# Performance work log

Measured on AMD Instinct MI355X. Metric: run time of the kernel, lower is better.

The kernel has to match this reference:

```python
import jax, jax.numpy as jnp
import numpy as np
from jax import lax

B, L, F = 32, 2048, 76   # batch, seq_len, feat_dim
H = 128                  # conv hidden channels
D = 128                  # prototype dim (last 1x1 conv)
P = 128                  # number of prototypes
CLASS_SIZE = 2


def setup_inputs() -> dict:
    key = jax.random.key(0)
    ks = jax.random.split(key, 8)
    w = lambda k, shape: jax.random.normal(k, shape, jnp.float32) * 0.05
    return {
        "x": jax.random.normal(ks[0], (B, L, F), jnp.float32),
        "W1": w(ks[1], (H, F, 5)), "b1": jnp.zeros((H,), jnp.float32),
        "W2": w(ks[2], (H, H, 5)), "b2": jnp.zeros((H,), jnp.float32),
        "W3": w(ks[3], (H, H, 5)), "b3": jnp.zeros((H,), jnp.float32),
        "Wo1": w(ks[4], (D, H)), "bo1": jnp.zeros((D,), jnp.float32),
        "Wo2": w(ks[5], (D, D)), "bo2": jnp.zeros((D,), jnp.float32),
        "prototypes": jax.random.uniform(ks[6], (P, D), jnp.float32),
        "protop_classes": jnp.concatenate([jnp.zeros(P // 2, jnp.int32), jnp.ones(P // 2, jnp.int32)]),
    }


def _conv1d_same(h, W, b):
    # h: (B, C, L), W: (O, C, K=5), symmetric padding 2 == torch padding=k//2
    y = lax.conv_general_dilated(h, W, window_strides=(1,), padding=[(2, 2)],
                                 dimension_numbers=("NCW", "OIW", "NCW"))
    return y + b[None, :, None]


def _maxpool2(h):
    return lax.reduce_window(h, -jnp.inf, lax.max, (1, 1, 2), (1, 1, 2), "VALID")


def reference(x, W1, b1, W2, b2, W3, b3, Wo1, bo1, Wo2, bo2, prototypes, protop_classes):
    h = jnp.transpose(x, (0, 2, 1))  # (B, F, L)
    for W, b in ((W1, b1), (W2, b2), (W3, b3)):
        h = _maxpool2(jax.nn.relu(_conv1d_same(h, W, b)))
    # 1x1 convs as channel matmuls
    h = jax.nn.relu(jnp.einsum("bcl,oc->bol", h, Wo1) + bo1[None, :, None])
    h = jax.nn.relu(jnp.einsum("bcl,oc->bol", h, Wo2) + bo2[None, :, None])
    f = jnp.transpose(h, (0, 2, 1))  # (B, Lp=256, D)
    # l2_conv via ||a-b||^2 = ||a||^2 - 2 a.b + ||b||^2 (same math, GEMM form)
    d2 = (jnp.sum(f * f, axis=-1, keepdims=True)
          - 2.0 * jnp.einsum("bld,pd->blp", f, prototypes)
          + jnp.sum(prototypes * prototypes, axis=-1))  # (B, Lp, P)
    dis = jnp.sqrt(jnp.maximum(d2, 1e-12))
    min_dis = jnp.min(dis, axis=1)  # (B, P): min over patches
    # dis2sim, 'log' activation
    sim = jnp.log((min_dis + 1.0) / (min_dis + 1e-4))
    # init_weights: last_layer.weight[i,j] = 1 if protop_classes[j]==i else -0.5
    lw = jnp.where(protop_classes[None, :] == jnp.arange(CLASS_SIZE)[:, None], 1.0, -0.5)
    out = jax.nn.sigmoid(sim @ lw.T)  # (B, CLASS_SIZE)
    return out, min_dis
```

## Files before the change

kernel.cpp:

```cpp
#include <hip/hip_runtime.h>
#include <cmath>


typedef __attribute__((ext_vector_type(8))) short short8;
typedef __attribute__((ext_vector_type(4))) float f32x4;

__device__ __forceinline__ unsigned short f2bf(float v) {
    union { float f; unsigned u; } x; x.f = v;
    unsigned r = x.u + 0x7fffu + ((x.u >> 16) & 1u);
    return (unsigned short)(r >> 16);
}
__device__ __forceinline__ float bf2f(unsigned short b) {
    union { unsigned u; float f; } x; x.u = ((unsigned)b) << 16;
    return x.f;
}

__device__ void pack_conv_w(int t, int total, const float* __restrict__ W, int C,
                            unsigned short* __restrict__ dst)
{
    if (t >= total) return;
    int lane = t & 63, rest = t >> 6;
    int mf = rest & 7; rest >>= 3;
    int kk = rest % 5, cc = rest / 5;
    int m = mf * 16 + (lane & 15);
    int cb = cc * 32 + (lane >> 4) * 8;
    unsigned short v[8];
#pragma unroll
    for (int j = 0; j < 8; ++j) {
        int c = cb + j;
        v[j] = (c < C) ? f2bf(W[((size_t)m * C + c) * 5 + kk]) : (unsigned short)0;
    }
    *(uint4*)&dst[(size_t)t * 8] = *(uint4*)v;
}

__device__ void pack_mat(int t, const float* __restrict__ M, unsigned short* __restrict__ dst)
{
    if (t >= 2048) return;
    int lane = t & 63, mf = (t >> 6) & 7, cc = t >> 9;
    int m = mf * 16 + (lane & 15);
    int c0 = cc * 32 + (lane >> 4) * 8;
    unsigned short v[8];
#pragma unroll
    for (int j = 0; j < 8; ++j) v[j] = f2bf(M[(size_t)m * 128 + c0 + j]);
    *(uint4*)&dst[(size_t)t * 8] = *(uint4*)v;
}

__global__ __launch_bounds__(256)
void prep_weights_kernel(const float* __restrict__ W1, const float* __restrict__ W2,
                         const float* __restrict__ W3, const float* __restrict__ Wo1,
                         const float* __restrict__ Wo2, const float* __restrict__ protos,
                         unsigned short* A1, unsigned short* A2, unsigned short* A3,
                         unsigned short* AW1, unsigned short* AW2, unsigned short* AP,
                         float* pn, unsigned* pm_bits, unsigned* cnt)
{
    int t = blockIdx.x * 256 + threadIdx.x;
    switch (blockIdx.y) {
    case 0: pack_conv_w(t, 7680,  W1, 76,  A1); break;
    case 1: pack_conv_w(t, 10240, W2, 128, A2); break;
    case 2: pack_conv_w(t, 10240, W3, 128, A3); break;
    case 3: pack_mat(t, Wo1, AW1); break;
    case 4: pack_mat(t, Wo2, AW2); break;
    case 5: pack_mat(t, protos, AP); break;
    case 6:
        if (t < 128) {
            float s = 0.f;
            for (int d = 0; d < 128; ++d) {
                float v = bf2f(f2bf(protos[(size_t)t * 128 + d]));
                s = fmaf(v, v, s);
            }
            pn[t] = s;
        }
        break;
    case 7:
        if (t < 4096)                    pm_bits[t] = 0x7F800000u;
        else if (cnt && t < 4128)        cnt[t - 4096] = 0u;
        break;
    }
}

template <int MF, int NJ, int NCC, int STRIDE, int ROWMAX>
__device__ __forceinline__ void conv_k(const unsigned short* __restrict__ Af,
                                       const unsigned short* __restrict__ sIn,
                                       int nbase, int mf0, int lane,
                                       f32x4 (&acc)[MF][NJ])
{
    const int lc = lane & 15;
    const int lk = (lane >> 4) * 8;
    constexpr int NSTEP = NCC * 5;
#pragma unroll
    for (int i = 0; i < MF; ++i)
#pragma unroll
        for (int j = 0; j < NJ; ++j) acc[i][j] = (f32x4){0.f, 0.f, 0.f, 0.f};

    short8 a_cur[MF], a_nxt[MF];
#pragma unroll
    for (int i = 0; i < MF; ++i)
        a_cur[i] = *(const short8*)&Af[(((size_t)mf0 + i) * 64 + lane) * 8];

#pragma unroll
    for (int step = 0; step < NSTEP; ++step) {
        const int kk = step % 5, cc = step / 5;
        if (step + 1 < NSTEP) {
#pragma unroll
            for (int i = 0; i < MF; ++i)
                a_nxt[i] = *(const short8*)&Af[(((size_t)(step + 1) * 8 + mf0 + i) * 64 + lane) * 8];
        }
        short8 bb[NJ];
#pragma unroll
        for (int j = 0; j < NJ; ++j) {
            int row = nbase + j * 16 + lc + kk;
            if (ROWMAX >= 0) row = min(row, ROWMAX);
            bb[j] = *(const short8*)&sIn[row * STRIDE + cc * 32 + lk];
        }
        __builtin_amdgcn_s_setprio(1);
#pragma unroll
        for (int j = 0; j < NJ; ++j)
#pragma unroll
            for (int i = 0; i < MF; ++i)
                acc[i][j] = __builtin_amdgcn_mfma_f32_16x16x32_bf16(a_cur[i], bb[j], acc[i][j], 0, 0, 0);
        __builtin_amdgcn_s_setprio(0);
#pragma unroll
        for (int i = 0; i < MF; ++i) a_cur[i] = a_nxt[i];
    }
}

__device__ __forceinline__ void gemm_head(const unsigned short* __restrict__ Af,
                                          const unsigned short* __restrict__ s_in,
                                          int mf0h, int lane, f32x4 (&acc)[2])
{
    const int lc = lane & 15;
    const int lk = (lane >> 4) * 8;
    acc[0] = (f32x4){0.f, 0.f, 0.f, 0.f};
    acc[1] = (f32x4){0.f, 0.f, 0.f, 0.f};
#pragma unroll
    for (int cc = 0; cc < 4; ++cc) {
        short8 a[2];
#pragma unroll
        for (int i = 0; i < 2; ++i)
            a[i] = *(const short8*)&Af[(((size_t)cc * 8 + mf0h + i) * 64 + lane) * 8];
        short8 bb = *(const short8*)&s_in[lc * 136 + cc * 32 + lk];
        __builtin_amdgcn_s_setprio(1);
#pragma unroll
        for (int i = 0; i < 2; ++i)
            acc[i] = __builtin_amdgcn_mfma_f32_16x16x32_bf16(a[i], bb, acc[i], 0, 0, 0);
        __builtin_amdgcn_s_setprio(0);
    }
}

__global__ __launch_bounds__(256, 4)
void mega_kernel(const float* __restrict__ x,
                 const unsigned short* __restrict__ A1, const float* __restrict__ b1,
                 const unsigned short* __restrict__ A2, const float* __restrict__ b2,
                 const unsigned short* __restrict__ A3, const float* __restrict__ b3,
                 const unsigned short* __restrict__ AW1, const float* __restrict__ bo1,
                 const unsigned short* __restrict__ AW2, const float* __restrict__ bo2,
                 const unsigned short* __restrict__ AP,  const float* __restrict__ pn,
                 unsigned* __restrict__ pm_bits, unsigned* __restrict__ cnt,
                 const int* __restrict__ classes, float* __restrict__ out)
{
    __shared__ __align__(16) unsigned short s_x[100 * 104];
    __shared__ __align__(16) unsigned short s_h1[44 * 136];
    __shared__ float s_cb[768];
    __shared__ float s_part[64];
    __shared__ unsigned s_last;
    unsigned short* s_h2 = s_x;
    unsigned short* s_f  = s_x + 2720;
    unsigned short* s_t1 = s_x + 4896;

    const int tid  = threadIdx.x;
    const int u    = blockIdx.x;
    const int b    = blockIdx.y;
    const int lane = tid & 63;
    const int wid  = tid >> 6;
    const int mg   = wid & 1;
    const int ng   = wid >> 1;
    const int mf0  = mg * 4;
    const int lc   = lane & 15;
    const int lq   = (lane >> 4) * 4;

    for (int i = tid; i < 768; i += 256) {
        const float* src = (i < 128) ? b1 : (i < 256) ? b2 : (i < 384) ? b3
                         : (i < 512) ? bo1 : (i < 640) ? bo2 : pn;
        s_cb[i] = src[i & 127];
    }

    const int xbase = 64 * u - 14;
    for (int idx = tid; idx < 100 * 24; idx += 256) {
        int pos = idx / 24, c0 = (idx % 24) * 4;
        int l = xbase + pos;
        unsigned short v[4] = {0, 0, 0, 0};
        if (c0 < 76 && l >= 0 && l < 2048) {
            float4 xv = *(const float4*)&x[((size_t)b * 2048 + l) * 76 + c0];
            v[0] = f2bf(xv.x); v[1] = f2bf(xv.y); v[2] = f2bf(xv.z); v[3] = f2bf(xv.w);
        }
        *(uint2*)&s_x[pos * 104 + c0] = *(uint2*)v;
    }
    __syncthreads();

    {
        f32x4 acc[4][3];
        conv_k<4, 3, 3, 104, -1>(A1, s_x, ng * 48, mf0, lane, acc);

#pragma unroll
        for (int i = 0; i < 4; ++i) {
            const int ch0 = (mf0 + i) * 16 + lq;
#pragma unroll
            for (int j = 0; j < 3; ++j) {
                const int nl = ng * 48 + j * 16 + lc;
                unsigned short pk[4];
#pragma unroll
                for (int r = 0; r < 4; ++r) {
                    float v = fmaxf(acc[i][j][r] + s_cb[ch0 + r], 0.f);
                    float o = __shfl_xor(v, 1);
                    pk[r] = f2bf(fmaxf(v, o));
                }
                if ((lc & 1) == 0) {
                    int rr = nl >> 1;
                    int jg = 32 * u - 6 + rr;
                    if (rr < 44) {
                        uint2 val = (jg >= 0 && jg < 1024) ? *(uint2*)pk : make_uint2(0u, 0u);
                        *(uint2*)&s_h1[rr * 136 + ch0] = val;
                    }
                }
            }
        }
    }
    __syncthreads();

    {
        if (tid < 136) ((uint4*)(s_f + 8 * 136))[tid] = make_uint4(0u, 0u, 0u, 0u);

        f32x4 acc[2][3];
        conv_k<2, 3, 4, 136, 43>(A2, s_h1, 0, wid * 2, lane, acc);

#pragma unroll
        for (int i = 0; i < 2; ++i) {
            const int ch0 = (wid * 2 + i) * 16 + lq;
#pragma unroll
            for (int j = 0; j < 3; ++j) {
                const int nl = j * 16 + lc;
                unsigned short pk[4];
#pragma unroll
                for (int r = 0; r < 4; ++r) {
                    float v = fmaxf(acc[i][j][r] + s_cb[128 + ch0 + r], 0.f);
                    float o = __shfl_xor(v, 1);
                    pk[r] = f2bf(fmaxf(v, o));
                }
                if ((lc & 1) == 0) {
                    int rr = nl >> 1;
                    int jg = 16 * u - 2 + rr;
                    if (rr < 20) {
                        uint2 val = (jg >= 0 && jg < 512) ? *(uint2*)pk : make_uint2(0u, 0u);
                        *(uint2*)&s_h2[rr * 136 + ch0] = val;
                    }
                }
            }
        }
    }
    __syncthreads();

    {
        f32x4 acc[2][1];
        conv_k<2, 1, 4, 136, -1>(A3, s_h2, 0, wid * 2, lane, acc);

#pragma unroll
        for (int i = 0; i < 2; ++i) {
            const int ch0 = (wid * 2 + i) * 16 + lq;
            unsigned short pk[4];
#pragma unroll
            for (int r = 0; r < 4; ++r) {
                float v = fmaxf(acc[i][0][r] + s_cb[256 + ch0 + r], 0.f);
                float o = __shfl_xor(v, 1);
                pk[r] = f2bf(fmaxf(v, o));
            }
            if ((lc & 1) == 0)
                *(uint2*)&s_f[(lc >> 1) * 136 + ch0] = *(uint2*)pk;
        }
    }
    __syncthreads();

    const int mf0h = wid * 2;
    f32x4 hacc[2];

    gemm_head(AW1, s_f, mf0h, lane, hacc);
#pragma unroll
    for (int i = 0; i < 2; ++i) {
        const int ch0 = (mf0h + i) * 16 + lq;
        unsigned short pk[4];
#pragma unroll
        for (int r = 0; r < 4; ++r)
            pk[r] = f2bf(fmaxf(hacc[i][r] + s_cb[384 + ch0 + r], 0.f));
        *(uint2*)&s_t1[lc * 136 + ch0] = *(uint2*)pk;
    }
    __syncthreads();

    gemm_head(AW2, s_t1, mf0h, lane, hacc);
    {
        float fnp = 0.f;
#pragma unroll
        for (int i = 0; i < 2; ++i) {
            const int ch0 = (mf0h + i) * 16 + lq;
            unsigned short pk[4];
#pragma unroll
            for (int r = 0; r < 4; ++r) {
                float v = fmaxf(hacc[i][r] + s_cb[512 + ch0 + r], 0.f);
                fnp = fmaf(v, v, fnp);
                pk[r] = f2bf(v);
            }
            *(uint2*)&s_f[lc * 136 + ch0] = *(uint2*)pk;
        }
        fnp += __shfl_xor(fnp, 16);
        fnp += __shfl_xor(fnp, 32);
        if (lane < 16) s_part[wid * 16 + lc] = fnp;
    }
    __syncthreads();

    gemm_head(AP, s_f, mf0h, lane, hacc);
    const float fn_l = s_part[lc] + s_part[16 + lc] + s_part[32 + lc] + s_part[48 + lc];

#pragma unroll
    for (int i = 0; i < 2; ++i) {
#pragma unroll
        for (int r = 0; r < 4; ++r) {
            const int p = (mf0h + i) * 16 + lq + r;
            float d2 = fn_l + s_cb[640 + p] - 2.f * hacc[i][r];
            float m = sqrtf(fmaxf(d2, 1e-12f));
#pragma unroll
            for (int s = 1; s < 8; s <<= 1)
                m = fminf(m, __shfl_xor(m, s));
            if (lc == 0)
                atomicMin(&pm_bits[(size_t)b * 128 + p], __float_as_uint(m));
        }
    }

    if (cnt) {
        __syncthreads();
        if (tid == 0) {
            __threadfence();
            s_last = atomicAdd(&cnt[b], 1u);
        }
        __syncthreads();
        if (s_last == 31u) {
            __threadfence();
            float* r0 = (float*)s_h1;
            float* r1 = r0 + 128;
            if (tid < 128) {
                unsigned mb = atomicOr(&pm_bits[(size_t)b * 128 + tid], 0u);
                float m = __uint_as_float(mb);
                out[64 + b * 128 + tid] = m;
                float sim = logf((m + 1.0f) / (m + 1e-4f));
                int c = classes[tid];
                r0[tid] = (c == 0) ? sim : -0.5f * sim;
                r1[tid] = (c == 1) ? sim : -0.5f * sim;
            }
            __syncthreads();
            for (int s = 64; s > 0; s >>= 1) {
                if (tid < s) { r0[tid] += r0[tid + s]; r1[tid] += r1[tid + s]; }
                __syncthreads();
            }
            if (tid == 0) {
                out[b * 2 + 0] = 1.f / (1.f + expf(-r0[0]));
                out[b * 2 + 1] = 1.f / (1.f + expf(-r1[0]));
            }
        }
    }
}

__global__ __launch_bounds__(128)
void finalize_kernel(const float* __restrict__ pm,
                     const int* __restrict__ classes,
                     float* __restrict__ out)
{
    __shared__ float r0[128], r1[128];
    const int b = blockIdx.x, p = threadIdx.x;
    float m = pm[(size_t)b * 128 + p];
    out[64 + b * 128 + p] = m;

    float sim = logf((m + 1.0f) / (m + 1e-4f));
    int cls = classes[p];
    r0[p] = (cls == 0) ? sim : -0.5f * sim;
    r1[p] = (cls == 1) ? sim : -0.5f * sim;
    __syncthreads();
    for (int s = 64; s > 0; s >>= 1) {
        if (p < s) { r0[p] += r0[p + s]; r1[p] += r1[p + s]; }
        __syncthreads();
    }
    if (p == 0) {
        out[b * 2 + 0] = 1.f / (1.f + expf(-r0[0]));
        out[b * 2 + 1] = 1.f / (1.f + expf(-r1[0]));
    }
}

extern "C" void kernel_launch(void* const* d_in, const int* in_sizes, int n_in,
                              void* d_out, int out_size, void* d_ws, size_t ws_size,
                              hipStream_t stream)
{
    (void)in_sizes; (void)n_in; (void)out_size;
    const float* x    = (const float*)d_in[0];
    const float* W1   = (const float*)d_in[1];
    const float* b1   = (const float*)d_in[2];
    const float* W2   = (const float*)d_in[3];
    const float* b2   = (const float*)d_in[4];
    const float* W3   = (const float*)d_in[5];
    const float* b3   = (const float*)d_in[6];
    const float* Wo1  = (const float*)d_in[7];
    const float* bo1  = (const float*)d_in[8];
    const float* Wo2  = (const float*)d_in[9];
    const float* bo2  = (const float*)d_in[10];
    const float* prot = (const float*)d_in[11];
    const int*   cls  = (const int*)d_in[12];
    float* out = (float*)d_out;

    char* ws = (char*)d_ws;
    unsigned short* A1  = (unsigned short*)(ws);
    unsigned short* A2  = (unsigned short*)(ws + 122880);
    unsigned short* A3  = (unsigned short*)(ws + 286720);
    unsigned short* AW1 = (unsigned short*)(ws + 450560);
    unsigned short* AW2 = (unsigned short*)(ws + 483328);
    unsigned short* AP  = (unsigned short*)(ws + 516096);
    float*          pn  = (float*)(ws + 548864);
    unsigned*       pm  = (unsigned*)(ws + 549376);
    const bool merged = (ws_size >= 565760u + 128u);
    unsigned*       cnt = merged ? (unsigned*)(ws + 565760) : nullptr;

    prep_weights_kernel<<<dim3(40, 8), 256, 0, stream>>>(W1, W2, W3, Wo1, Wo2, prot,
                                                         A1, A2, A3, AW1, AW2, AP, pn, pm, cnt);
    mega_kernel<<<dim3(32, 32), 256, 0, stream>>>(x, A1, b1, A2, b2, A3, b3,
                                                  AW1, bo1, AW2, bo2, AP, pn, pm, cnt,
                                                  cls, out);
    if (!merged)
        finalize_kernel<<<32, 128, 0, stream>>>((const float*)pm, cls, out);
}
```

Before: 152.6 us.

## Retile conv1 warps over channels only and drop A-fragment prefetch and setprio

Conv1 work is split so each wave handles 2 channel fragments across all 96 positions (MF=2, NJ=6) instead of 4 channel fragments across half the positions. This halves per-wave weight-fragment traffic for conv1 but doubles LDS B reads per MFMA. The software double-buffering of A fragments and the s_setprio hints are removed, and the cc loop is no longer fully unrolled, which lowers register pressure but may expose global-load latency.

```diff
diff --git a/kernel.cpp b/kernel.cpp
--- a/kernel.cpp
+++ b/kernel.cpp
@@ -86,41 +86,32 @@
 {
     const int lc = lane & 15;
     const int lk = (lane >> 4) * 8;
-    constexpr int NSTEP = NCC * 5;
 #pragma unroll
     for (int i = 0; i < MF; ++i)
 #pragma unroll
         for (int j = 0; j < NJ; ++j) acc[i][j] = (f32x4){0.f, 0.f, 0.f, 0.f};
 
-    short8 a_cur[MF], a_nxt[MF];
-#pragma unroll
-    for (int i = 0; i < MF; ++i)
-        a_cur[i] = *(const short8*)&Af[(((size_t)mf0 + i) * 64 + lane) * 8];
-
-#pragma unroll
-    for (int step = 0; step < NSTEP; ++step) {
-        const int kk = step % 5, cc = step / 5;
-        if (step + 1 < NSTEP) {
+    for (int cc = 0; cc < NCC; ++cc) {
+#pragma unroll
+        for (int kk = 0; kk < 5; ++kk) {
+            const int step = cc * 5 + kk;
+            short8 a[MF];
 #pragma unroll
             for (int i = 0; i < MF; ++i)
-                a_nxt[i] = *(const short8*)&Af[(((size_t)(step + 1) * 8 + mf0 + i) * 64 + lane) * 8];
-        }
-        short8 bb[NJ];
-#pragma unroll
-        for (int j = 0; j < NJ; ++j) {
-            int row = nbase + j * 16 + lc + kk;
-            if (ROWMAX >= 0) row = min(row, ROWMAX);
-            bb[j] = *(const short8*)&sIn[row * STRIDE + cc * 32 + lk];
-        }
-        __builtin_amdgcn_s_setprio(1);
-#pragma unroll
-        for (int j = 0; j < NJ; ++j)
-#pragma unroll
-            for (int i = 0; i < MF; ++i)
-                acc[i][j] = __builtin_amdgcn_mfma_f32_16x16x32_bf16(a_cur[i], bb[j], acc[i][j], 0, 0, 0);
-        __builtin_amdgcn_s_setprio(0);
-#pragma unroll
-        for (int i = 0; i < MF; ++i) a_cur[i] = a_nxt[i];
+                a[i] = *(const short8*)&Af[(((size_t)step * 8 + mf0 + i) * 64 + lane) * 8];
+            short8 bb[NJ];
+#pragma unroll
+            for (int j = 0; j < NJ; ++j) {
+                int row = nbase + j * 16 + lc + kk;
+                if (ROWMAX >= 0) row = min(row, ROWMAX);
+                bb[j] = *(const short8*)&sIn[row * STRIDE + cc * 32 + lk];
+            }
+#pragma unroll
+            for (int j = 0; j < NJ; ++j)
+#pragma unroll
+                for (int i = 0; i < MF; ++i)
+                    acc[i][j] = __builtin_amdgcn_mfma_f32_16x16x32_bf16(a[i], bb[j], acc[i][j], 0, 0, 0);
+        }
     }
 }
 
@@ -139,11 +130,9 @@
         for (int i = 0; i < 2; ++i)
             a[i] = *(const short8*)&Af[(((size_t)cc * 8 + mf0h + i) * 64 + lane) * 8];
         short8 bb = *(const short8*)&s_in[lc * 136 + cc * 32 + lk];
-        __builtin_amdgcn_s_setprio(1);
 #pragma unroll
         for (int i = 0; i < 2; ++i)
             acc[i] = __builtin_amdgcn_mfma_f32_16x16x32_bf16(a[i], bb, acc[i], 0, 0, 0);
-        __builtin_amdgcn_s_setprio(0);
     }
 }
 
@@ -172,9 +161,7 @@
     const int b    = blockIdx.y;
     const int lane = tid & 63;
     const int wid  = tid >> 6;
-    const int mg   = wid & 1;
-    const int ng   = wid >> 1;
-    const int mf0  = mg * 4;
+    const int mf0  = wid * 2;
     const int lc   = lane & 15;
     const int lq   = (lane >> 4) * 4;
 
@@ -198,15 +185,15 @@
     __syncthreads();
 
     {
-        f32x4 acc[4][3];
-        conv_k<4, 3, 3, 104, -1>(A1, s_x, ng * 48, mf0, lane, acc);
-
-#pragma unroll
-        for (int i = 0; i < 4; ++i) {
+        f32x4 acc[2][6];
+        conv_k<2, 6, 3, 104, -1>(A1, s_x, 0, mf0, lane, acc);
+
+#pragma unroll
+        for (int i = 0; i < 2; ++i) {
             const int ch0 = (mf0 + i) * 16 + lq;
 #pragma unroll
-            for (int j = 0; j < 3; ++j) {
-                const int nl = ng * 48 + j * 16 + lc;
+            for (int j = 0; j < 6; ++j) {
+                const int nl = j * 16 + lc;
                 unsigned short pk[4];
 #pragma unroll
                 for (int r = 0; r < 4; ++r) {
@@ -231,11 +218,11 @@
         if (tid < 136) ((uint4*)(s_f + 8 * 136))[tid] = make_uint4(0u, 0u, 0u, 0u);
 
         f32x4 acc[2][3];
-        conv_k<2, 3, 4, 136, 43>(A2, s_h1, 0, wid * 2, lane, acc);
+        conv_k<2, 3, 4, 136, 43>(A2, s_h1, 0, mf0, lane, acc);
 
 #pragma unroll
         for (int i = 0; i < 2; ++i) {
-            const int ch0 = (wid * 2 + i) * 16 + lq;
+            const int ch0 = (mf0 + i) * 16 + lq;
 #pragma unroll
             for (int j = 0; j < 3; ++j) {
                 const int nl = j * 16 + lc;
@@ -261,11 +248,11 @@
 
     {
         f32x4 acc[2][1];
-        conv_k<2, 1, 4, 136, -1>(A3, s_h2, 0, wid * 2, lane, acc);
+        conv_k<2, 1, 4, 136, -1>(A3, s_h2, 0, mf0, lane, acc);
 
 #pragma unroll
         for (int i = 0; i < 2; ++i) {
-            const int ch0 = (wid * 2 + i) * 16 + lq;
+            const int ch0 = (mf0 + i) * 16 + lq;
             unsigned short pk[4];
 #pragma unroll
             for (int r = 0; r < 4; ++r) {
@@ -279,13 +266,12 @@
     }
     __syncthreads();
 
-    const int mf0h = wid * 2;
     f32x4 hacc[2];
 
-    gemm_head(AW1, s_f, mf0h, lane, hacc);
+    gemm_head(AW1, s_f, mf0, lane, hacc);
 #pragma unroll
     for (int i = 0; i < 2; ++i) {
-        const int ch0 = (mf0h + i) * 16 + lq;
+        const int ch0 = (mf0 + i) * 16 + lq;
         unsigned short pk[4];
 #pragma unroll
         for (int r = 0; r < 4; ++r)
@@ -294,12 +280,12 @@
     }
     __syncthreads();
 
-    gemm_head(AW2, s_t1, mf0h, lane, hacc);
+    gemm_head(AW2, s_t1, mf0, lane, hacc);
     {
         float fnp = 0.f;
 #pragma unroll
         for (int i = 0; i < 2; ++i) {
-            const int ch0 = (mf0h + i) * 16 + lq;
+            const int ch0 = (mf0 + i) * 16 + lq;
             unsigned short pk[4];
 #pragma unroll
             for (int r = 0; r < 4; ++r) {
@@ -315,14 +301,14 @@
     }
     __syncthreads();
 
-    gemm_head(AP, s_f, mf0h, lane, hacc);
+    gemm_head(AP, s_f, mf0, lane, hacc);
     const float fn_l = s_part[lc] + s_part[16 + lc] + s_part[32 + lc] + s_part[48 + lc];
 
 #pragma unroll
     for (int i = 0; i < 2; ++i) {
 #pragma unroll
         for (int r = 0; r < 4; ++r) {
-            const int p = (mf0h + i) * 16 + lq + r;
+            const int p = (mf0 + i) * 16 + lq + r;
             float d2 = fn_l + s_cb[640 + p] - 2.f * hacc[i][r];
             float m = sqrtf(fmaxf(d2, 1e-12f));
 #pragma unroll
```

After: 148.4 us. 2.7% less time.
